# Kernel tuning notes

Measured on AMD Instinct MI355X. Metric: run time of the kernel, lower is better.

## Reference

```python
import jax, jax.numpy as jnp
import numpy as np

B, S, D, H = 4, 4096, 1024, 16
HD = D // H  # head_dim = 64

def setup_inputs() -> dict:
    key = jax.random.key(0)
    ks = jax.random.split(key, 9)
    sc = 1.0 / np.sqrt(D)
    return {
        "x": jax.random.normal(ks[0], (B, S, D), dtype=jnp.float32),
        "q_w": jax.random.normal(ks[1], (D, D), dtype=jnp.float32) * sc,
        "q_b": jax.random.normal(ks[2], (D,), dtype=jnp.float32) * 0.01,
        "k_w": jax.random.normal(ks[3], (D, D), dtype=jnp.float32) * sc,
        "k_b": jax.random.normal(ks[4], (D,), dtype=jnp.float32) * 0.01,
        "v_w": jax.random.normal(ks[5], (D, D), dtype=jnp.float32) * sc,
        "v_b": jax.random.normal(ks[6], (D,), dtype=jnp.float32) * 0.01,
        "o_w": jax.random.normal(ks[7], (D, D), dtype=jnp.float32) * sc,
        "o_b": jax.random.normal(ks[8], (D,), dtype=jnp.float32) * 0.01,
    }

def reference(x, q_w, q_b, k_w, k_b, v_w, v_b, o_w, o_b):
    b, s, _ = x.shape
    # Linear projections (torch Linear: x @ W.T + b), split heads
    q = (x @ q_w.T + q_b).reshape(b, s, H, HD)
    k = (x @ k_w.T + k_b).reshape(b, s, H, HD)
    v = (x @ v_w.T + v_b).reshape(b, s, H, HD)
    # ReLU feature map on q and k
    q = jax.nn.relu(q)
    k = jax.nn.relu(k)
    # Non-causal linear attention: kv state then query readout
    kv = jnp.einsum('bshd,bshe->bhde', k, v)   # [B,H,HD,HD]
    out = jnp.einsum('bqhd,bhde->bqhe', q, kv)  # [B,S,H,HD]
    out = out.reshape(b, s, D)
    return out @ o_w.T + o_b
```

## Files before the change

### kernel.cpp

```cpp
#include <hip/hip_runtime.h>

typedef unsigned short ushort_t;
typedef __attribute__((ext_vector_type(8))) __bf16 bf16x8;
typedef __attribute__((ext_vector_type(8))) unsigned short us8;
typedef __attribute__((ext_vector_type(4))) float f32x4;

#define GLOAD_LDS16(gp, lp)                                                              \
  __builtin_amdgcn_global_load_lds(                                                     \
      (const __attribute__((address_space(1))) unsigned int*)(gp),                      \
      (__attribute__((address_space(3))) unsigned int*)(lp), 16, 0, 0)

#define MEMFENCE() asm volatile("" ::: "memory")
#define SBARRIER()                          \
  do {                                      \
    MEMFENCE();                             \
    __builtin_amdgcn_s_barrier();           \
    MEMFENCE();                             \
  } while (0)
#define WAIT_VM2() asm volatile("s_waitcnt vmcnt(2)" ::: "memory")
#define WAIT_VM0() asm volatile("s_waitcnt vmcnt(0)" ::: "memory")
#define WAIT_LGKM0P() asm volatile("s_waitcnt lgkmcnt(0)" ::: "memory")
#define WAIT_LGKM8() asm volatile("s_waitcnt lgkmcnt(8)" ::: "memory")

__device__ __forceinline__ ushort_t f2bf(float f) {
  unsigned u = __builtin_bit_cast(unsigned, f);
  u += 0x7fffu + ((u >> 16) & 1u);
  return (ushort_t)(u >> 16);
}
__device__ __forceinline__ float bf2f(ushort_t h) {
  return __builtin_bit_cast(float, (unsigned)h << 16);
}

__global__ __launch_bounds__(256) void k_f32_to_bf16(const float* __restrict__ src,
                                                     ushort_t* __restrict__ dst, int n) {
  int i = (blockIdx.x * 256 + threadIdx.x) * 4;
  if (i >= n) return;
  float4 v = *reinterpret_cast<const float4*>(src + i);
  ushort4 o;
  o.x = f2bf(v.x); o.y = f2bf(v.y); o.z = f2bf(v.z); o.w = f2bf(v.w);
  *reinterpret_cast<ushort4*>(dst + i) = o;
}

__global__ __launch_bounds__(256) void k_pack_w4(const float* __restrict__ w0,
                                                 const float* __restrict__ w1,
                                                 const float* __restrict__ w2,
                                                 const float* __restrict__ w3,
                                                 ushort_t* __restrict__ dst) {
  const int blk = blockIdx.x;
  const int wsel = blk >> 10;
  const float* src = wsel == 0 ? w0 : wsel == 1 ? w1 : wsel == 2 ? w2 : w3;
  const int off = (blk & 1023) * 1024 + threadIdx.x * 4;
  float4 v = *reinterpret_cast<const float4*>(src + off);
  ushort4 o;
  o.x = f2bf(v.x); o.y = f2bf(v.y); o.z = f2bf(v.z); o.w = f2bf(v.w);
  *reinterpret_cast<ushort4*>(dst + wsel * 1048576 + off) = o;
}

__global__ __launch_bounds__(256) void k_pack_bias(const float* __restrict__ q_b,
                                                   const float* __restrict__ k_b,
                                                   const float* __restrict__ v_b,
                                                   float* __restrict__ biasq) {
  int i = blockIdx.x * 256 + threadIdx.x;
  const float* s = i < 1024 ? q_b : (i < 2048 ? k_b : v_b);
  biasq[i] = s[i & 1023];
}


__device__ __forceinline__ void stage_half(const ushort_t* __restrict__ g, int ld, int kt,
                                           ushort_t* slot, int w, int lane) {
  const int swz = ((lane & 7) ^ (lane >> 3)) * 8;
#pragma unroll
  for (int l = 0; l < 2; l++) {
    int row = l * 64 + w * 8 + (lane >> 3);
    GLOAD_LDS16(g + (long)row * ld + kt + swz, slot + l * 4096 + w * 512);
  }
}

__device__ __forceinline__ bf16x8 read_frag(const ushort_t* slot, int row, int kbyte) {
  int byte = row * 128 + (kbyte ^ ((row & 7) << 4));
  return *reinterpret_cast<const bf16x8*>(reinterpret_cast<const char*>(slot) + byte);
}

template <bool OUT_F32>
__global__ __launch_bounds__(512, 2) void k_gemm256(
    const ushort_t* __restrict__ A, int lda, long strideA,
    const ushort_t* __restrict__ Bw, int ldb, long strideB,
    const float* __restrict__ bias, int relu_lim,
    void* __restrict__ Cout, int ldc, long strideC, int K) {
  __shared__ ushort_t lds[65536];
  const int t = threadIdx.x;
  const int lane = t & 63;
  const int w = t >> 6;
  const int wm = w >> 2, wn = w & 3;
  const int z = blockIdx.z;

  const int nx = gridDim.x;
  const int nwg = nx * gridDim.y;
  const int lin = blockIdx.x + blockIdx.y * nx;
  const int q8 = nwg >> 3;
  const int s = (lin & 7) * q8 + (lin >> 3);
  const long rowBase = (long)(s / nx) * 256;
  const long colBase = (long)(s % nx) * 256;

  const ushort_t* Ap = A + z * strideA + rowBase * lda;
  const ushort_t* Bp = Bw + z * strideB + colBase * ldb;

#define SLOT(buf, isB, half) (lds + (buf) * 32768 + (isB) * 16384 + (half) * 8192)
#define STAGE(gb, ld, kt, buf, isB, half) stage_half((gb), (ld), (kt), SLOT(buf, isB, half), w, lane)

  f32x4 acc[8][4];
#pragma unroll
  for (int mi = 0; mi < 8; mi++)
#pragma unroll
    for (int ni = 0; ni < 4; ni++) acc[mi][ni] = (f32x4){0.f, 0.f, 0.f, 0.f};
  bf16x8 Ar[4][2], Br[4][2];
  const int fr = lane & 15;
  const int kb = (lane >> 4) * 16;

#define LOADA(buf, miB)                                                             \
  do {                                                                              \
    const ushort_t* sl = SLOT(buf, 0, wm);                                          \
    _Pragma("unroll") for (int mi = 0; mi < 4; mi++)                                \
        _Pragma("unroll") for (int ks = 0; ks < 2; ks++)                            \
            Ar[mi][ks] = read_frag(sl, (miB + mi) * 16 + fr, ks * 64 + kb);         \
  } while (0)
#define LOADB(buf, ns)                                                              \
  do {                                                                              \
    const ushort_t* sl = SLOT(buf, 1, wn >> 1);                                     \
    _Pragma("unroll") for (int nj = 0; nj < 2; nj++)                                \
        _Pragma("unroll") for (int ks = 0; ks < 2; ks++)                            \
            Br[(ns) * 2 + nj][ks] =                                                 \
                read_frag(sl, (wn & 1) * 64 + ((ns) * 2 + nj) * 16 + fr, ks * 64 + kb); \
  } while (0)
#define MFMA16(miB, ns)                                                             \
  do {                                                                              \
    _Pragma("unroll") for (int ks = 0; ks < 2; ks++)                                \
        _Pragma("unroll") for (int mi = 0; mi < 4; mi++)                            \
            _Pragma("unroll") for (int nj = 0; nj < 2; nj++)                        \
                acc[(miB) + mi][(ns) * 2 + nj] = __builtin_amdgcn_mfma_f32_16x16x32_bf16( \
                    Ar[mi][ks], Br[(ns) * 2 + nj][ks], acc[(miB) + mi][(ns) * 2 + nj], 0, 0, 0); \
  } while (0)

  const ushort_t* Ap1 = Ap + 128 * (long)lda;
  const ushort_t* Bp1 = Bp + 128 * (long)ldb;

  STAGE(Ap, lda, 0, 0, 0, 0);
  STAGE(Bp, ldb, 0, 0, 1, 0);
  STAGE(Ap1, lda, 0, 0, 0, 1);
  STAGE(Bp1, ldb, 0, 0, 1, 1);
  STAGE(Ap, lda, 64, 1, 0, 0);
  WAIT_VM2();
  SBARRIER();

  const int NT2 = K >> 7;
  for (int it = 0; it < NT2; it++) {
    const int kt = it << 7;
    const int ktb = kt + 64;
    const int ktn = (kt + 128 < K) ? kt + 128 : K - 64;
    const int ktn2 = (kt + 192 < K) ? kt + 192 : K - 64;

    LOADA(0, 0); LOADB(0, 0);
    STAGE(Bp, ldb, ktb, 1, 1, 0);
    WAIT_LGKM8();
    SBARRIER();
    WAIT_LGKM0P();
    __builtin_amdgcn_s_setprio(1); MFMA16(0, 0); __builtin_amdgcn_s_setprio(0);
    LOADB(0, 1);
    STAGE(Ap1, lda, ktb, 1, 0, 1);
    SBARRIER();
    WAIT_LGKM0P();
    __builtin_amdgcn_s_setprio(1); MFMA16(0, 1); __builtin_amdgcn_s_setprio(0);
    LOADA(0, 4);
    STAGE(Bp1, ldb, ktb, 1, 1, 1);
    SBARRIER();
    WAIT_LGKM0P();
    __builtin_amdgcn_s_setprio(1); MFMA16(4, 0); __builtin_amdgcn_s_setprio(0);
    STAGE(Ap, lda, ktn, 0, 0, 0);
    SBARRIER();
    __builtin_amdgcn_s_setprio(1); MFMA16(4, 1); __builtin_amdgcn_s_setprio(0);
    WAIT_VM2();
    SBARRIER();
    LOADA(1, 0); LOADB(1, 0);
    STAGE(Bp, ldb, ktn, 0, 1, 0);
    WAIT_LGKM8();
    SBARRIER();
    WAIT_LGKM0P();
    __builtin_amdgcn_s_setprio(1); MFMA16(0, 0); __builtin_amdgcn_s_setprio(0);
    LOADB(1, 1);
    STAGE(Ap1, lda, ktn, 0, 0, 1);
    SBARRIER();
    WAIT_LGKM0P();
    __builtin_amdgcn_s_setprio(1); MFMA16(0, 1); __builtin_amdgcn_s_setprio(0);
    LOADA(1, 4);
    STAGE(Bp1, ldb, ktn, 0, 1, 1);
    SBARRIER();
    WAIT_LGKM0P();
    __builtin_amdgcn_s_setprio(1); MFMA16(4, 0); __builtin_amdgcn_s_setprio(0);
    STAGE(Ap, lda, ktn2, 1, 0, 0);
    SBARRIER();
    __builtin_amdgcn_s_setprio(1); MFMA16(4, 1); __builtin_amdgcn_s_setprio(0);
    WAIT_VM2();
    SBARRIER();
  }

  WAIT_VM0();
  SBARRIER();
  {
    float* sl = reinterpret_cast<float*>(lds) + w * 2048;
    const int rowQ = (lane >> 4) * 4;
    float bv[4];
#pragma unroll
    for (int ni = 0; ni < 4; ni++) bv[ni] = bias[(int)colBase + wn * 64 + ni * 16 + fr];
    const int rr = lane >> 2;
    const int cq = (lane & 3) * 16;
#pragma unroll
    for (int mi = 0; mi < 8; mi++) {
#pragma unroll
      for (int ni = 0; ni < 4; ni++) {
        const bool doRelu = ((int)colBase + wn * 64 + ni * 16 + fr) < relu_lim;
#pragma unroll
        for (int r = 0; r < 4; r++) {
          float v = acc[mi][ni][r] + bv[ni];
          if (doRelu) v = fmaxf(v, 0.f);
          sl[(rowQ + r) * 68 + ni * 16 + fr] = v;
        }
      }
      asm volatile("s_waitcnt lgkmcnt(0)" ::: "memory");
      __builtin_amdgcn_sched_barrier(0);
      float4 v0 = *reinterpret_cast<const float4*>(&sl[rr * 68 + cq]);
      float4 v1 = *reinterpret_cast<const float4*>(&sl[rr * 68 + cq + 4]);
      float4 v2 = *reinterpret_cast<const float4*>(&sl[rr * 68 + cq + 8]);
      float4 v3 = *reinterpret_cast<const float4*>(&sl[rr * 68 + cq + 12]);
      const long row = rowBase + wm * 128 + mi * 16 + rr;
      const long gc = colBase + wn * 64 + cq;
      if (OUT_F32) {
        float* dst = (float*)Cout + z * strideC + row * (long)ldc + gc;
        *reinterpret_cast<float4*>(dst) = v0;
        *reinterpret_cast<float4*>(dst + 4) = v1;
        *reinterpret_cast<float4*>(dst + 8) = v2;
        *reinterpret_cast<float4*>(dst + 12) = v3;
      } else {
        ushort_t* dst = (ushort_t*)Cout + z * strideC + row * (long)ldc + gc;
        us8 o0, o1;
        o0[0] = f2bf(v0.x); o0[1] = f2bf(v0.y); o0[2] = f2bf(v0.z); o0[3] = f2bf(v0.w);
        o0[4] = f2bf(v1.x); o0[5] = f2bf(v1.y); o0[6] = f2bf(v1.z); o0[7] = f2bf(v1.w);
        o1[0] = f2bf(v2.x); o1[1] = f2bf(v2.y); o1[2] = f2bf(v2.z); o1[3] = f2bf(v2.w);
        o1[4] = f2bf(v3.x); o1[5] = f2bf(v3.y); o1[6] = f2bf(v3.z); o1[7] = f2bf(v3.w);
        *reinterpret_cast<us8*>(dst) = o0;
        *reinterpret_cast<us8*>(dst + 8) = o1;
      }
      asm volatile("s_waitcnt lgkmcnt(0)" ::: "memory");
    }
  }
#undef SLOT
#undef STAGE
#undef LOADA
#undef LOADB
#undef MFMA16
}

__global__ __launch_bounds__(64) void k_kv_partial(const ushort_t* __restrict__ qkv,
                                                   float* __restrict__ partial) {
  const int bh = blockIdx.x;
  const int chunk = blockIdx.y;
  const int b = bh >> 4, h = bh & 15;
  const int t = threadIdx.x;
  const int d0 = (t >> 2) * 4;
  const int e0 = (t & 3) * 16;
  __shared__ float kk[16][64];
  __shared__ float vv[16][64];
  float acc[4][16];
#pragma unroll
  for (int di = 0; di < 4; di++)
#pragma unroll
    for (int j = 0; j < 16; j++) acc[di][j] = 0.f;

  const long rowbase = (long)b * 4096 + (long)chunk * 128;
  for (int it = 0; it < 8; it++) {
    __syncthreads();
#pragma unroll
    for (int rep = 0; rep < 4; rep++) {
      int idx = rep * 64 + t;
      int row = idx >> 4, c4 = (idx & 15) * 4;
      long m = rowbase + it * 16 + row;
      ushort4 kr = *reinterpret_cast<const ushort4*>(&qkv[m * 3072 + 1024 + h * 64 + c4]);
      ushort4 vr = *reinterpret_cast<const ushort4*>(&qkv[m * 3072 + 2048 + h * 64 + c4]);
      float4 kf = make_float4(bf2f(kr.x), bf2f(kr.y), bf2f(kr.z), bf2f(kr.w));
      float4 vf = make_float4(bf2f(vr.x), bf2f(vr.y), bf2f(vr.z), bf2f(vr.w));
      *reinterpret_cast<float4*>(&kk[row][c4]) = kf;
      *reinterpret_cast<float4*>(&vv[row][c4]) = vf;
    }
    __syncthreads();
#pragma unroll
    for (int ss = 0; ss < 16; ss++) {
      const float4 kq = *reinterpret_cast<const float4*>(&kk[ss][d0]);
#pragma unroll
      for (int jj = 0; jj < 4; jj++) {
        const float4 vq = *reinterpret_cast<const float4*>(&vv[ss][e0 + jj * 4]);
        acc[0][jj * 4 + 0] = fmaf(kq.x, vq.x, acc[0][jj * 4 + 0]);
        acc[0][jj * 4 + 1] = fmaf(kq.x, vq.y, acc[0][jj * 4 + 1]);
        acc[0][jj * 4 + 2] = fmaf(kq.x, vq.z, acc[0][jj * 4 + 2]);
        acc[0][jj * 4 + 3] = fmaf(kq.x, vq.w, acc[0][jj * 4 + 3]);
        acc[1][jj * 4 + 0] = fmaf(kq.y, vq.x, acc[1][jj * 4 + 0]);
        acc[1][jj * 4 + 1] = fmaf(kq.y, vq.y, acc[1][jj * 4 + 1]);
        acc[1][jj * 4 + 2] = fmaf(kq.y, vq.z, acc[1][jj * 4 + 2]);
        acc[1][jj * 4 + 3] = fmaf(kq.y, vq.w, acc[1][jj * 4 + 3]);
        acc[2][jj * 4 + 0] = fmaf(kq.z, vq.x, acc[2][jj * 4 + 0]);
        acc[2][jj * 4 + 1] = fmaf(kq.z, vq.y, acc[2][jj * 4 + 1]);
        acc[2][jj * 4 + 2] = fmaf(kq.z, vq.z, acc[2][jj * 4 + 2]);
        acc[2][jj * 4 + 3] = fmaf(kq.z, vq.w, acc[2][jj * 4 + 3]);
        acc[3][jj * 4 + 0] = fmaf(kq.w, vq.x, acc[3][jj * 4 + 0]);
        acc[3][jj * 4 + 1] = fmaf(kq.w, vq.y, acc[3][jj * 4 + 1]);
        acc[3][jj * 4 + 2] = fmaf(kq.w, vq.z, acc[3][jj * 4 + 2]);
        acc[3][jj * 4 + 3] = fmaf(kq.w, vq.w, acc[3][jj * 4 + 3]);
      }
    }
  }
  float* dst = partial + ((long)chunk * 64 + bh) * 4096;
#pragma unroll
  for (int di = 0; di < 4; di++)
#pragma unroll
    for (int jj = 0; jj < 4; jj++) {
      float4 o = make_float4(acc[di][jj * 4], acc[di][jj * 4 + 1], acc[di][jj * 4 + 2],
                             acc[di][jj * 4 + 3]);
      *reinterpret_cast<float4*>(&dst[(d0 + di) * 64 + e0 + jj * 4]) = o;
    }
}

__global__ __launch_bounds__(256) void k_kv_reduce(const float* __restrict__ partial,
                                                   float* __restrict__ kv) {
  int i4 = (blockIdx.x * 256 + threadIdx.x) * 4;
  float4 s = make_float4(0.f, 0.f, 0.f, 0.f);
#pragma unroll
  for (int c = 0; c < 32; c++) {
    float4 p = *reinterpret_cast<const float4*>(&partial[(long)c * 262144 + i4]);
    s.x += p.x; s.y += p.y; s.z += p.z; s.w += p.w;
  }
  *reinterpret_cast<float4*>(&kv[i4]) = s;
}

__global__ __launch_bounds__(256) void k_fuse_w(const float* __restrict__ kv,
                                                const ushort_t* __restrict__ ow,
                                                ushort_t* __restrict__ qkv) {
  const int nt = blockIdx.x;
  const int h = blockIdx.y;
  const int b = blockIdx.z;
  const int t = threadIdx.x;
  const int nn = t >> 2;
  const int d0 = (t & 3) * 16;
  __shared__ float kvt[64][68];
  __shared__ ushort_t ows[64][68];
  const float* kvsrc = kv + (long)(b * 16 + h) * 4096;
  const int n0 = nt * 64;
#pragma unroll
  for (int rep = 0; rep < 16; rep++) {
    int lin = rep * 256 + t;
    int d = lin >> 6, e = lin & 63;
    kvt[e][d] = kvsrc[d * 64 + e];
  }
#pragma unroll
  for (int rep = 0; rep < 4; rep++) {
    int lin = rep * 256 + t;
    int r = lin >> 4, c4 = (lin & 15) * 4;
    *reinterpret_cast<ushort4*>(&ows[r][c4]) =
        *reinterpret_cast<const ushort4*>(&ow[(long)(n0 + r) * 1024 + h * 64 + c4]);
  }
  __syncthreads();
  float acc[16];
#pragma unroll
  for (int j = 0; j < 16; j++) acc[j] = 0.f;
  for (int e = 0; e < 64; e++) {
    float own = bf2f(ows[nn][e]);
#pragma unroll
    for (int jj = 0; jj < 4; jj++) {
      const float4 kq = *reinterpret_cast<const float4*>(&kvt[e][d0 + jj * 4]);
      acc[jj * 4 + 0] = fmaf(own, kq.x, acc[jj * 4 + 0]);
      acc[jj * 4 + 1] = fmaf(own, kq.y, acc[jj * 4 + 1]);
      acc[jj * 4 + 2] = fmaf(own, kq.z, acc[jj * 4 + 2]);
      acc[jj * 4 + 3] = fmaf(own, kq.w, acc[jj * 4 + 3]);
    }
  }
  ushort_t* dst = qkv + (long)(b * 1024 + n0 + nn) * 3072 + 1024 + h * 64 + d0;
#pragma unroll
  for (int jj = 0; jj < 4; jj++) {
    ushort4 o;
    o.x = f2bf(acc[jj * 4 + 0]); o.y = f2bf(acc[jj * 4 + 1]);
    o.z = f2bf(acc[jj * 4 + 2]); o.w = f2bf(acc[jj * 4 + 3]);
    *reinterpret_cast<ushort4*>(dst + jj * 4) = o;
  }
}

extern "C" void kernel_launch(void* const* d_in, const int* in_sizes, int n_in, void* d_out,
                              int out_size, void* d_ws, size_t ws_size, hipStream_t stream) {
  const float* x   = (const float*)d_in[0];
  const float* q_w = (const float*)d_in[1];
  const float* q_b = (const float*)d_in[2];
  const float* k_w = (const float*)d_in[3];
  const float* k_b = (const float*)d_in[4];
  const float* v_w = (const float*)d_in[5];
  const float* v_b = (const float*)d_in[6];
  const float* o_w = (const float*)d_in[7];
  const float* o_b = (const float*)d_in[8];
  float* out = (float*)d_out;

  const int D = 1024, M = 16384;
  char* ws = (char*)d_ws;
  ushort_t* xb    = (ushort_t*)(ws);
  ushort_t* wqkv  = (ushort_t*)(ws + 33554432);
  ushort_t* owb   = (ushort_t*)(ws + 39845888);
  float*    biasq = (float*)(ws + 41943040);
  ushort_t* qkv   = (ushort_t*)(ws + 41955328);
  float* partial = (float*)(ws);
  float* kvbuf   = (float*)(ws + 33554432);

  k_f32_to_bf16<<<16384, 256, 0, stream>>>(x, xb, M * D);
  k_pack_w4<<<4096, 256, 0, stream>>>(q_w, k_w, v_w, o_w, wqkv);
  k_pack_bias<<<12, 256, 0, stream>>>(q_b, k_b, v_b, biasq);

  k_gemm256<false><<<dim3(12, 64, 1), 512, 0, stream>>>(xb, 1024, 0, wqkv, 1024, 0,
                                                        biasq, 2048, qkv, 3072, 0, 1024);
  k_kv_partial<<<dim3(64, 32), 64, 0, stream>>>(qkv, partial);
  k_kv_reduce<<<256, 256, 0, stream>>>(partial, kvbuf);
  k_fuse_w<<<dim3(16, 16, 4), 256, 0, stream>>>(kvbuf, owb, qkv);
  k_gemm256<true><<<dim3(4, 16, 4), 512, 0, stream>>>(
      qkv, 3072, (long)4096 * 3072, qkv + 1024, 3072, (long)1024 * 3072,
      o_b, 0, out, 1024, (long)4096 * 1024, 1024);
}
```

Baseline: 235.8 us.

## Deepen GEMM prefetch schedule and reduce kv partials in-block across four waves

The GEMM main loop is rescheduled so each B half-tile is prefetched one phase earlier. The full A fragment set (8 rows) is held in registers, so LDS reads for both A halves happen before the MFMAs. The vmcnt wait is raised to 4 to allow more loads in flight. The kv partial kernel now uses 256-thread blocks where four waves each process a 128-row chunk and reduce through shared memory, cutting the partial buffer and the reduce pass from 32 chunks to 8. This costs more registers for A fragments and more LDS in the kv kernel, which may lower occupancy.

```diff
diff --git a/kernel.cpp b/kernel.cpp
--- a/kernel.cpp
+++ b/kernel.cpp
@@ -17,7 +17,7 @@
     __builtin_amdgcn_s_barrier();           \
     MEMFENCE();                             \
   } while (0)
-#define WAIT_VM2() asm volatile("s_waitcnt vmcnt(2)" ::: "memory")
+#define WAIT_VM4() asm volatile("s_waitcnt vmcnt(4)" ::: "memory")
 #define WAIT_VM0() asm volatile("s_waitcnt vmcnt(0)" ::: "memory")
 #define WAIT_LGKM0P() asm volatile("s_waitcnt lgkmcnt(0)" ::: "memory")
 #define WAIT_LGKM8() asm volatile("s_waitcnt lgkmcnt(8)" ::: "memory")
@@ -113,7 +113,8 @@
   for (int mi = 0; mi < 8; mi++)
 #pragma unroll
     for (int ni = 0; ni < 4; ni++) acc[mi][ni] = (f32x4){0.f, 0.f, 0.f, 0.f};
-  bf16x8 Ar[4][2], Br[4][2];
+  bf16x8 Ar8[8][2];
+  bf16x8 Br[4][2];
   const int fr = lane & 15;
   const int kb = (lane >> 4) * 16;
 
@@ -122,7 +123,7 @@
     const ushort_t* sl = SLOT(buf, 0, wm);                                          \
     _Pragma("unroll") for (int mi = 0; mi < 4; mi++)                                \
         _Pragma("unroll") for (int ks = 0; ks < 2; ks++)                            \
-            Ar[mi][ks] = read_frag(sl, (miB + mi) * 16 + fr, ks * 64 + kb);         \
+            Ar8[(miB) + mi][ks] = read_frag(sl, ((miB) + mi) * 16 + fr, ks * 64 + kb); \
   } while (0)
 #define LOADB(buf, ns)                                                              \
   do {                                                                              \
@@ -138,7 +139,7 @@
         _Pragma("unroll") for (int mi = 0; mi < 4; mi++)                            \
             _Pragma("unroll") for (int nj = 0; nj < 2; nj++)                        \
                 acc[(miB) + mi][(ns) * 2 + nj] = __builtin_amdgcn_mfma_f32_16x16x32_bf16( \
-                    Ar[mi][ks], Br[(ns) * 2 + nj][ks], acc[(miB) + mi][(ns) * 2 + nj], 0, 0, 0); \
+                    Ar8[(miB) + mi][ks], Br[(ns) * 2 + nj][ks], acc[(miB) + mi][(ns) * 2 + nj], 0, 0, 0); \
   } while (0)
 
   const ushort_t* Ap1 = Ap + 128 * (long)lda;
@@ -149,57 +150,56 @@
   STAGE(Ap1, lda, 0, 0, 0, 1);
   STAGE(Bp1, ldb, 0, 0, 1, 1);
   STAGE(Ap, lda, 64, 1, 0, 0);
-  WAIT_VM2();
+  STAGE(Bp, ldb, 64, 1, 1, 0);
+  WAIT_VM4();
   SBARRIER();
 
   const int NT2 = K >> 7;
   for (int it = 0; it < NT2; it++) {
     const int kt = it << 7;
     const int ktb = kt + 64;
-    const int ktn = (kt + 128 < K) ? kt + 128 : K - 64;
+    const int ktn  = (kt + 128 < K) ? kt + 128 : K - 64;
     const int ktn2 = (kt + 192 < K) ? kt + 192 : K - 64;
 
     LOADA(0, 0); LOADB(0, 0);
-    STAGE(Bp, ldb, ktb, 1, 1, 0);
+    STAGE(Ap1, lda, ktb, 1, 0, 1);
     WAIT_LGKM8();
     SBARRIER();
     WAIT_LGKM0P();
     __builtin_amdgcn_s_setprio(1); MFMA16(0, 0); __builtin_amdgcn_s_setprio(0);
-    LOADB(0, 1);
-    STAGE(Ap1, lda, ktb, 1, 0, 1);
+    LOADA(0, 4); LOADB(0, 1);
+    STAGE(Bp1, ldb, ktb, 1, 1, 1);
+    WAIT_LGKM8();
     SBARRIER();
     WAIT_LGKM0P();
     __builtin_amdgcn_s_setprio(1); MFMA16(0, 1); __builtin_amdgcn_s_setprio(0);
-    LOADA(0, 4);
-    STAGE(Bp1, ldb, ktb, 1, 1, 1);
-    SBARRIER();
-    WAIT_LGKM0P();
+    STAGE(Ap, lda, ktn, 0, 0, 0);
+    SBARRIER();
     __builtin_amdgcn_s_setprio(1); MFMA16(4, 0); __builtin_amdgcn_s_setprio(0);
-    STAGE(Ap, lda, ktn, 0, 0, 0);
+    STAGE(Bp, ldb, ktn, 0, 1, 0);
     SBARRIER();
     __builtin_amdgcn_s_setprio(1); MFMA16(4, 1); __builtin_amdgcn_s_setprio(0);
-    WAIT_VM2();
+    WAIT_VM4();
     SBARRIER();
     LOADA(1, 0); LOADB(1, 0);
-    STAGE(Bp, ldb, ktn, 0, 1, 0);
+    STAGE(Ap1, lda, ktn, 0, 0, 1);
     WAIT_LGKM8();
     SBARRIER();
     WAIT_LGKM0P();
     __builtin_amdgcn_s_setprio(1); MFMA16(0, 0); __builtin_amdgcn_s_setprio(0);
-    LOADB(1, 1);
-    STAGE(Ap1, lda, ktn, 0, 0, 1);
+    LOADA(1, 4); LOADB(1, 1);
+    STAGE(Bp1, ldb, ktn, 0, 1, 1);
+    WAIT_LGKM8();
     SBARRIER();
     WAIT_LGKM0P();
     __builtin_amdgcn_s_setprio(1); MFMA16(0, 1); __builtin_amdgcn_s_setprio(0);
-    LOADA(1, 4);
-    STAGE(Bp1, ldb, ktn, 0, 1, 1);
-    SBARRIER();
-    WAIT_LGKM0P();
+    STAGE(Ap, lda, ktn2, 1, 0, 0);
+    SBARRIER();
     __builtin_amdgcn_s_setprio(1); MFMA16(4, 0); __builtin_amdgcn_s_setprio(0);
-    STAGE(Ap, lda, ktn2, 1, 0, 0);
+    STAGE(Bp, ldb, ktn2, 1, 1, 0);
     SBARRIER();
     __builtin_amdgcn_s_setprio(1); MFMA16(4, 1); __builtin_amdgcn_s_setprio(0);
-    WAIT_VM2();
+    WAIT_VM4();
     SBARRIER();
   }
 
@@ -259,44 +259,46 @@
 #undef MFMA16
 }
 
-__global__ __launch_bounds__(64) void k_kv_partial(const ushort_t* __restrict__ qkv,
-                                                   float* __restrict__ partial) {
+__global__ __launch_bounds__(256) void k_kv_partial(const ushort_t* __restrict__ qkv,
+                                                    float* __restrict__ partial) {
   const int bh = blockIdx.x;
   const int chunk = blockIdx.y;
   const int b = bh >> 4, h = bh & 15;
   const int t = threadIdx.x;
-  const int d0 = (t >> 2) * 4;
-  const int e0 = (t & 3) * 16;
-  __shared__ float kk[16][64];
-  __shared__ float vv[16][64];
+  const int w = t >> 6, lane = t & 63;
+  const int d0 = (lane >> 2) * 4;
+  const int e0 = (lane & 3) * 16;
+  __shared__ float smem[16384];
+  float* kk = smem + w * 2048;
+  float* vv = smem + w * 2048 + 1024;
   float acc[4][16];
 #pragma unroll
   for (int di = 0; di < 4; di++)
 #pragma unroll
     for (int j = 0; j < 16; j++) acc[di][j] = 0.f;
 
-  const long rowbase = (long)b * 4096 + (long)chunk * 128;
-  for (int it = 0; it < 8; it++) {
+  const long rowbase = (long)b * 4096 + (long)chunk * 512 + (long)w * 128;
+  for (int itr = 0; itr < 8; itr++) {
     __syncthreads();
 #pragma unroll
     for (int rep = 0; rep < 4; rep++) {
-      int idx = rep * 64 + t;
+      int idx = rep * 64 + lane;
       int row = idx >> 4, c4 = (idx & 15) * 4;
-      long m = rowbase + it * 16 + row;
+      long m = rowbase + itr * 16 + row;
       ushort4 kr = *reinterpret_cast<const ushort4*>(&qkv[m * 3072 + 1024 + h * 64 + c4]);
       ushort4 vr = *reinterpret_cast<const ushort4*>(&qkv[m * 3072 + 2048 + h * 64 + c4]);
       float4 kf = make_float4(bf2f(kr.x), bf2f(kr.y), bf2f(kr.z), bf2f(kr.w));
       float4 vf = make_float4(bf2f(vr.x), bf2f(vr.y), bf2f(vr.z), bf2f(vr.w));
-      *reinterpret_cast<float4*>(&kk[row][c4]) = kf;
-      *reinterpret_cast<float4*>(&vv[row][c4]) = vf;
+      *reinterpret_cast<float4*>(&kk[row * 64 + c4]) = kf;
+      *reinterpret_cast<float4*>(&vv[row * 64 + c4]) = vf;
     }
     __syncthreads();
 #pragma unroll
     for (int ss = 0; ss < 16; ss++) {
-      const float4 kq = *reinterpret_cast<const float4*>(&kk[ss][d0]);
+      const float4 kq = *reinterpret_cast<const float4*>(&kk[ss * 64 + d0]);
 #pragma unroll
       for (int jj = 0; jj < 4; jj++) {
-        const float4 vq = *reinterpret_cast<const float4*>(&vv[ss][e0 + jj * 4]);
+        const float4 vq = *reinterpret_cast<const float4*>(&vv[ss * 64 + e0 + jj * 4]);
         acc[0][jj * 4 + 0] = fmaf(kq.x, vq.x, acc[0][jj * 4 + 0]);
         acc[0][jj * 4 + 1] = fmaf(kq.x, vq.y, acc[0][jj * 4 + 1]);
         acc[0][jj * 4 + 2] = fmaf(kq.x, vq.z, acc[0][jj * 4 + 2]);
@@ -316,15 +318,35 @@
       }
     }
   }
-  float* dst = partial + ((long)chunk * 64 + bh) * 4096;
+  __syncthreads();
 #pragma unroll
   for (int di = 0; di < 4; di++)
 #pragma unroll
-    for (int jj = 0; jj < 4; jj++) {
-      float4 o = make_float4(acc[di][jj * 4], acc[di][jj * 4 + 1], acc[di][jj * 4 + 2],
-                             acc[di][jj * 4 + 3]);
-      *reinterpret_cast<float4*>(&dst[(d0 + di) * 64 + e0 + jj * 4]) = o;
-    }
+    for (int j4 = 0; j4 < 4; j4++)
+      *reinterpret_cast<float4*>(&smem[(w * 64 + lane) * 64 + di * 16 + j4 * 4]) =
+          make_float4(acc[di][j4 * 4], acc[di][j4 * 4 + 1], acc[di][j4 * 4 + 2],
+                      acc[di][j4 * 4 + 3]);
+  __syncthreads();
+  const int u = (t >> 4) * 4 + (t & 3);
+  const int di = (t >> 2) & 3;
+  float4 r0 = {0, 0, 0, 0}, r1 = {0, 0, 0, 0}, r2 = {0, 0, 0, 0}, r3 = {0, 0, 0, 0};
+#pragma unroll
+  for (int ww = 0; ww < 4; ww++) {
+    const float* base = &smem[(ww * 64 + u) * 64 + di * 16];
+    float4 a0 = *reinterpret_cast<const float4*>(base);
+    float4 a1 = *reinterpret_cast<const float4*>(base + 4);
+    float4 a2 = *reinterpret_cast<const float4*>(base + 8);
+    float4 a3 = *reinterpret_cast<const float4*>(base + 12);
+    r0.x += a0.x; r0.y += a0.y; r0.z += a0.z; r0.w += a0.w;
+    r1.x += a1.x; r1.y += a1.y; r1.z += a1.z; r1.w += a1.w;
+    r2.x += a2.x; r2.y += a2.y; r2.z += a2.z; r2.w += a2.w;
+    r3.x += a3.x; r3.y += a3.y; r3.z += a3.z; r3.w += a3.w;
+  }
+  float* dst = partial + ((long)chunk * 64 + bh) * 4096 + t * 16;
+  *reinterpret_cast<float4*>(dst) = r0;
+  *reinterpret_cast<float4*>(dst + 4) = r1;
+  *reinterpret_cast<float4*>(dst + 8) = r2;
+  *reinterpret_cast<float4*>(dst + 12) = r3;
 }
 
 __global__ __launch_bounds__(256) void k_kv_reduce(const float* __restrict__ partial,
@@ -332,7 +354,7 @@
   int i4 = (blockIdx.x * 256 + threadIdx.x) * 4;
   float4 s = make_float4(0.f, 0.f, 0.f, 0.f);
 #pragma unroll
-  for (int c = 0; c < 32; c++) {
+  for (int c = 0; c < 8; c++) {
     float4 p = *reinterpret_cast<const float4*>(&partial[(long)c * 262144 + i4]);
     s.x += p.x; s.y += p.y; s.z += p.z; s.w += p.w;
   }
@@ -419,7 +441,7 @@
 
   k_gemm256<false><<<dim3(12, 64, 1), 512, 0, stream>>>(xb, 1024, 0, wqkv, 1024, 0,
                                                         biasq, 2048, qkv, 3072, 0, 1024);
-  k_kv_partial<<<dim3(64, 32), 64, 0, stream>>>(qkv, partial);
+  k_kv_partial<<<dim3(64, 8), 256, 0, stream>>>(qkv, partial);
   k_kv_reduce<<<256, 256, 0, stream>>>(partial, kvbuf);
   k_fuse_w<<<dim3(16, 16, 4), 256, 0, stream>>>(kvbuf, owb, qkv);
   k_gemm256<true><<<dim3(4, 16, 4), 512, 0, stream>>>(
```

After: 282.4 us. +19.7%, slower.
